# Kernel optimization log

Hardware: AMD Instinct MI355X
Metric: run time of the kernel (lower is better)

The kernel has to match this reference:

```python
import jax, jax.numpy as jnp
import numpy as np

B, N, D, T, L = 16, 64, 4, 40, 10
H, K = 128, 4
E = N * (N - 1)


def setup_inputs() -> dict:
    key = jax.random.key(0)
    ks = jax.random.split(key, 24)
    s = 0.05
    off = np.ones((N, N)) - np.eye(N)
    recv, send = np.where(off)  # rel_rec one-hot of recv, rel_send one-hot of send
    p = {}
    p["data"] = jax.random.normal(ks[0], (B, N, D, T), jnp.float32)
    p["rel_type"] = jax.random.uniform(ks[1], (B, E, K), dtype=jnp.float32)
    p["msg_W1"] = jax.random.normal(ks[2], (K, 2 * H, H), jnp.float32) * s
    p["msg_b1"] = jnp.zeros((K, H), jnp.float32)
    p["msg_W2"] = jax.random.normal(ks[3], (K, H, H), jnp.float32) * s
    p["msg_b2"] = jnp.zeros((K, H), jnp.float32)
    p["Wr_h"] = jax.random.normal(ks[4], (H, H), jnp.float32) * s
    p["Wi_h"] = jax.random.normal(ks[5], (H, H), jnp.float32) * s
    p["Wh_h"] = jax.random.normal(ks[6], (H, H), jnp.float32) * s
    p["Wr_in"] = jax.random.normal(ks[7], (D, H), jnp.float32) * s
    p["br_in"] = jnp.zeros((H,), jnp.float32)
    p["Wi_in"] = jax.random.normal(ks[8], (D, H), jnp.float32) * s
    p["bi_in"] = jnp.zeros((H,), jnp.float32)
    p["Wn_in"] = jax.random.normal(ks[9], (D, H), jnp.float32) * s
    p["bn_in"] = jnp.zeros((H,), jnp.float32)
    p["Wo1"] = jax.random.normal(ks[10], (H, H), jnp.float32) * s
    p["bo1"] = jnp.zeros((H,), jnp.float32)
    p["Wo2"] = jax.random.normal(ks[11], (H, H), jnp.float32) * s
    p["bo2"] = jnp.zeros((H,), jnp.float32)
    p["Wo3"] = jax.random.normal(ks[12], (H, D), jnp.float32) * s
    p["bo3"] = jnp.zeros((D,), jnp.float32)
    p["recv_idx"] = jnp.asarray(recv, jnp.int32)
    p["send_idx"] = jnp.asarray(send, jnp.int32)
    return p


def _forward(data, rel_type, msg_W1, msg_b1, msg_W2, msg_b2, Wr_h, Wi_h, Wh_h,
             Wr_in, br_in, Wi_in, bi_in, Wn_in, bn_in,
             Wo1, bo1, Wo2, bo2, Wo3, bo3, recv_idx, send_idx):
    inputs = jnp.transpose(data, (0, 3, 1, 2))  # [B,T,N,D]
    Bv = inputs.shape[0]

    def single_step(ins, hidden):
        # gather == matmul with one-hot rel_send / rel_rec
        pre_msg = jnp.concatenate([hidden[:, send_idx], hidden[:, recv_idx]], axis=-1)  # [B,E,2H]
        m = jnp.tanh(jnp.einsum('bef,kfh->bkeh', pre_msg, msg_W1) + msg_b1[None, :, None, :])
        m = jnp.tanh(jnp.einsum('bkeh,khg->bkeg', m, msg_W2) + msg_b2[None, :, None, :])
        # sum over edge types weighted by rel_type, normalized by num edge types
        all_msgs = jnp.einsum('bkeh,bek->beh', m, rel_type) / K
        # scatter-add to receivers == rel_rec^T matmul; normalized by n_in_node
        agg = jnp.zeros((Bv, N, H), all_msgs.dtype).at[:, recv_idx].add(all_msgs) / D
        r = jax.nn.sigmoid(ins @ Wr_in + br_in + agg @ Wr_h)
        i = jax.nn.sigmoid(ins @ Wi_in + bi_in + agg @ Wi_h)
        n = jnp.tanh(ins @ Wn_in + bn_in + r * (agg @ Wh_h))
        hidden = (1.0 - i) * n + i * hidden
        y = jax.nn.relu(hidden @ Wo1 + bo1)
        y = jax.nn.relu(y @ Wo2 + bo2)
        pred = ins + y @ Wo3 + bo3
        return pred, hidden

    inputs_pad = jnp.concatenate([inputs, jnp.zeros((Bv, L, N, D), inputs.dtype)], axis=1)
    xs_t = jnp.transpose(inputs_pad, (1, 0, 2, 3))  # [T+L,B,N,D]

    def scan_fn(carry, xs):
        hidden, prev = carry
        step, x_t = xs
        ins = jnp.where(step < T, x_t, prev)  # burn-in then closed-loop
        pred, hidden = single_step(ins, hidden)
        return (hidden, pred), pred

    init = (jnp.zeros((Bv, N, H), jnp.float32), jnp.zeros((Bv, N, D), jnp.float32))
    _, preds = jax.lax.scan(scan_fn, init, (jnp.arange(T + L), xs_t))
    preds = jnp.transpose(preds, (1, 2, 3, 0))  # [B,N,D,T+L]
    return preds[..., -L:]


def reference(data, rel_type, msg_W1, msg_b1, msg_W2, msg_b2, Wr_h, Wi_h, Wh_h,
              Wr_in, br_in, Wi_in, bi_in, Wn_in, bn_in,
              Wo1, bo1, Wo2, bo2, Wo3, bo3, recv_idx, send_idx):
    return _forward(data, rel_type, msg_W1, msg_b1, msg_W2, msg_b2, Wr_h, Wi_h, Wh_h,
                    Wr_in, br_in, Wi_in, bi_in, Wn_in, bn_in,
                    Wo1, bo1, Wo2, bo2, Wo3, bo3, recv_idx, send_idx)
```

## Files before the change

kernel.cpp:

```cpp
#include <hip/hip_runtime.h>
#include <hip/hip_bf16.h>
#include <math.h>

#define Bb 16
#define Nn 64
#define Dd 4
#define Tt 40
#define Ll 10
#define Hh 128
#define Kk 4
#define Ee (Nn*(Nn-1))
#define BNH (Bb*Nn*Hh)
#define SIGMA 2.8853900817779268f

typedef __attribute__((ext_vector_type(8))) short short8;
typedef __attribute__((ext_vector_type(4))) float f32x4;

#define AS1 __attribute__((address_space(1)))
#define AS3 __attribute__((address_space(3)))

__device__ __forceinline__ float tanhE(float y){
    float e = __builtin_amdgcn_exp2f(y);
    float r = __builtin_amdgcn_rcpf(e + 1.0f);
    return fmaf(-2.0f, r, 1.0f);
}
__device__ __forceinline__ float tanh_fast(float x){ return tanhE(SIGMA * x); }
__device__ __forceinline__ float sigmoid_fast(float x){
    return __builtin_amdgcn_rcpf(1.0f + __expf(-x));
}
__device__ __forceinline__ unsigned short f2bf(float x){
    unsigned int u = __float_as_uint(x);
    return (unsigned short)((u + 0x7FFFu + ((u >> 16) & 1u)) >> 16);
}
__device__ __forceinline__ unsigned int pack_bf2(float lo, float hi){
    union { __hip_bfloat162 h; unsigned int u; } cv;
    cv.h = __float22bfloat162_rn(make_float2(lo, hi));
    return cv.u;
}
__device__ __forceinline__ void g2lds16(const void* g, void* l){
    __builtin_amdgcn_global_load_lds((const AS1 unsigned int*)g,
                                     (AS3 unsigned int*)l, 16, 0, 0);
}

__global__ void __launch_bounds__(256) kW2f(const float* __restrict__ W2,
                                            const float* __restrict__ b2,
                                            unsigned short* __restrict__ W2f,
                                            float* __restrict__ b2l){
    if (blockIdx.x == 32){
        int i = threadIdx.x;
        b2l[i]       = SIGMA * b2[i];
        b2l[i + 256] = SIGMA * b2[i + 256];
        return;
    }
    int t    = blockIdx.x * 256 + threadIdx.x;
    int lane = t & 63;
    int nt   = (t >> 6) & 7;
    int kc   = (t >> 9) & 3;
    int k    = (t >> 11) & 3;
    int col  = nt * 16 + (lane & 15);
    int fb   = kc * 32 + (lane >> 4) * 8;
    unsigned int w[4];
#pragma unroll
    for (int p = 0; p < 4; ++p){
        unsigned short lo = f2bf(W2[(k*Hh + fb + 2*p    )*Hh + col]);
        unsigned short hi = f2bf(W2[(k*Hh + fb + 2*p + 1)*Hh + col]);
        w[p] = (unsigned int)lo | ((unsigned int)hi << 16);
    }
    ((uint4*)W2f)[t] = make_uint4(w[0], w[1], w[2], w[3]);
}

__global__ void __launch_bounds__(256) kW1f(const float* __restrict__ W1,
                                            unsigned short* __restrict__ W1f){
    int t    = blockIdx.x * 256 + threadIdx.x;
    int lane = t & 63;
    int nt   = (t >> 6) & 7;
    int kc   = (t >> 9) & 3;
    int s    = t >> 11;
    int col  = nt * 16 + (lane & 15);
    int fb   = kc * 32 + (lane >> 4) * 8;
    unsigned int w[4];
#pragma unroll
    for (int p = 0; p < 4; ++p){
        unsigned short lo = f2bf(W1[(size_t)(s*Hh + fb + 2*p    )*Hh + col]);
        unsigned short hi = f2bf(W1[(size_t)(s*Hh + fb + 2*p + 1)*Hh + col]);
        w[p] = (unsigned int)lo | ((unsigned int)hi << 16);
    }
    ((uint4*)W1f)[t] = make_uint4(w[0], w[1], w[2], w[3]);
}

__global__ void __launch_bounds__(256) kInit(const float* __restrict__ b1,
                                             float* __restrict__ Sf,
                                             float* __restrict__ Rr){
    int i = blockIdx.x*256 + threadIdx.x;
    Sf[i] = 0.0f;
    Rr[i] = SIGMA * b1[((i >> 13) & 3)*Hh + (i & 127)];
}

__global__ void __launch_bounds__(256) kA(const unsigned short* __restrict__ hbf,
                                          const unsigned short* __restrict__ W1f,
                                          const float* __restrict__ b1,
                                          float* __restrict__ Sf,
                                          float* __restrict__ Rr){
    const int blk   = blockIdx.x;
    const int bk    = blk & 63;
    const int b     = bk >> 2;
    const int k     = bk & 3;
    const int inner = blk >> 6;
    const int sr    = inner >> 1;
    const int mh    = inner & 1;
    const int s     = k*2 + sr;
    const int tid  = threadIdx.x;
    const int wave = tid >> 6;
    const int lane = tid & 63;
    const int nt0  = wave * 2;

    const short8* hv = (const short8*)hbf;
    const short8* wv = (const short8*)W1f;

    short8 a[2][4], bf[2][4];
#pragma unroll
    for (int m = 0; m < 2; ++m)
#pragma unroll
        for (int kc = 0; kc < 4; ++kc)
            a[m][kc] = hv[((size_t)((b*4 + mh*2 + m)*4) + kc)*64 + lane];
#pragma unroll
    for (int n = 0; n < 2; ++n)
#pragma unroll
        for (int kc = 0; kc < 4; ++kc)
            bf[n][kc] = wv[((size_t)(s*4 + kc)*8 + nt0 + n)*64 + lane];

    f32x4 acc[2][2];
#pragma unroll
    for (int m = 0; m < 2; ++m){ acc[m][0] = (f32x4)0.0f; acc[m][1] = (f32x4)0.0f; }

#pragma unroll
    for (int kc = 0; kc < 4; ++kc)
#pragma unroll
        for (int m = 0; m < 2; ++m){
            acc[m][0] = __builtin_amdgcn_mfma_f32_16x16x32_bf16(a[m][kc], bf[0][kc], acc[m][0], 0, 0, 0);
            acc[m][1] = __builtin_amdgcn_mfma_f32_16x16x32_bf16(a[m][kc], bf[1][kc], acc[m][1], 0, 0, 0);
        }

    const int col = lane & 15;
    const int r0  = (lane >> 4) << 2;
#pragma unroll
    for (int n = 0; n < 2; ++n){
        const int h  = (nt0 + n)*16 + col;
        const float bv = (sr == 1) ? b1[k*Hh + h] : 0.0f;
#pragma unroll
        for (int m = 0; m < 2; ++m){
            const int Mt = mh*2 + m;
#pragma unroll
            for (int r = 0; r < 4; ++r){
                const int node = Mt*16 + r0 + r;
                const float v = SIGMA*(acc[m][n][r] + bv);
                if (sr == 0)
                    Sf[((size_t)((b*4+k)*16 + (h>>3)))*512 + node*8 + (h&7)] = v;
                else
                    Rr[((size_t)((b*4+k)*64 + node))*128 + h] = v;
            }
        }
    }
}

__global__ void __launch_bounds__(512, 2) kB(const float* __restrict__ Sf,
                                             const float* __restrict__ Rr,
                                             const unsigned short* __restrict__ W2f,
                                             const float* __restrict__ b2l,
                                             const float* __restrict__ rel,
                                             float* __restrict__ aggp){
    __shared__ unsigned short w2s[32*512];
    __shared__ float sfs[8192];
    __shared__ float rrs[8*Hh];
    __shared__ float rel_s[8][64];
    __shared__ float b2s[Hh];

    const int blk  = blockIdx.x;
    const int k    = blk & 3;
    const int no   = (blk >> 2) & 7;
    const int b    = blk >> 5;
    const int tid  = threadIdx.x;
    const int wave = tid >> 6;
    const int lane = tid & 63;

    {
        const uint4* src = (const uint4*)(W2f + (size_t)k*16384);
        uint4* dst = (uint4*)w2s;
#pragma unroll
        for (int i = 0; i < 4; ++i)
            g2lds16(src + tid + i*512, dst + tid + i*512);
    }
    {
        const char* srcB = (const char*)(Sf + (size_t)((b*4 + k)*16)*512);
        char* dstB = (char*)sfs;
#pragma unroll
        for (int i = 0; i < 4; ++i){
            int p = i*8192 + tid*16;
            int g = p ^ (((p >> 11) & 7) << 4);
            g2lds16(srcB + g, dstB + p);
        }
    }
    if (tid < 256){
        const uint4* src = (const uint4*)(Rr + (size_t)((b*4 + k)*64 + no*8)*128);
        g2lds16(src + tid, (uint4*)rrs + tid);
    }
    {
        int g = tid >> 6, s = tid & 63;
        int n = no*8 + g;
        float w = 0.0f;
        if (s != n){
            int e = s - (s > n);
            w = rel[(b*Ee + n*63 + e)*Kk + k];
        }
        rel_s[g][s] = w;
    }
    if (tid < 128) b2s[tid] = b2l[k*Hh + tid];
    __syncthreads();

    const int n     = no*8 + wave;
    const int fo    = lane >> 4;
    const int srow  = lane & 15;
    const char* sfsB = (const char*)sfs;
    const float* rrw = rrs + wave*Hh;
    const short8* w2v = (const short8*)w2s;
    const float* relw = rel_s[wave];

    const int colb  = lane & 15;
    const int rbase = (lane >> 4) << 2;

    float aggacc[8];
#pragma unroll
    for (int nt = 0; nt < 8; ++nt) aggacc[nt] = 0.0f;

#pragma unroll 1
    for (int st = 0; st < 4; ++st){
        short8 a[4];
#pragma unroll
        for (int kc = 0; kc < 4; ++kc){
            const int fg = kc*4 + fo;
            const int A  = fg*2048 + (st*16 + srow)*32;
            const int sw = (fg & 7) << 4;
            float4 s0 = *(const float4*)(sfsB + (A ^ sw));
            float4 s1 = *(const float4*)(sfsB + ((A + 16) ^ sw));
            const float4* rp = (const float4*)(rrw + fg*8);
            float4 r0 = rp[0], r1 = rp[1];
            union { short8 v; unsigned int u[4]; } av;
            av.u[0] = pack_bf2(tanhE(s0.x+r0.x), tanhE(s0.y+r0.y));
            av.u[1] = pack_bf2(tanhE(s0.z+r0.z), tanhE(s0.w+r0.w));
            av.u[2] = pack_bf2(tanhE(s1.x+r1.x), tanhE(s1.y+r1.y));
            av.u[3] = pack_bf2(tanhE(s1.z+r1.z), tanhE(s1.w+r1.w));
            a[kc] = av.v;
        }

        f32x4 acc[8];
#pragma unroll
        for (int nt = 0; nt < 8; ++nt) acc[nt] = (f32x4)0.0f;
#pragma unroll
        for (int kc = 0; kc < 4; ++kc){
#pragma unroll
            for (int nt = 0; nt < 8; ++nt){
                short8 bfr = w2v[(kc*8 + nt)*64 + lane];
                acc[nt] = __builtin_amdgcn_mfma_f32_16x16x32_bf16(a[kc], bfr, acc[nt], 0, 0, 0);
            }
        }

#pragma unroll
        for (int nt = 0; nt < 8; ++nt){
            float bv = b2s[nt*16 + colb];
            float s = 0.0f;
#pragma unroll
            for (int r = 0; r < 4; ++r)
                s = fmaf(relw[st*16 + rbase + r], tanhE(fmaf(SIGMA, acc[nt][r], bv)), s);
            s += __shfl_xor(s, 16);
            s += __shfl_xor(s, 32);
            aggacc[nt] += s;
        }
    }

    if (lane < 16){
#pragma unroll
        for (int nt = 0; nt < 8; ++nt)
            aggp[(size_t)k*BNH + (size_t)(b*64 + n)*Hh + nt*16 + lane] = aggacc[nt];
    }
}

__global__ void __launch_bounds__(128) kC(const float* __restrict__ data,
                                          const float* __restrict__ aggp,
                                          float* __restrict__ hidden,
                                          float* __restrict__ prevpred,
                                          unsigned short* __restrict__ hbf,
                                          const float* __restrict__ Wr_in, const float* __restrict__ br_in,
                                          const float* __restrict__ Wi_in, const float* __restrict__ bi_in,
                                          const float* __restrict__ Wn_in, const float* __restrict__ bn_in,
                                          const float* __restrict__ Wr_h,  const float* __restrict__ Wi_h,
                                          const float* __restrict__ Wh_h,
                                          const float* __restrict__ Wo1,   const float* __restrict__ bo1,
                                          const float* __restrict__ Wo2,   const float* __restrict__ bo2,
                                          const float* __restrict__ Wo3,   const float* __restrict__ bo3,
                                          float* __restrict__ out, int t){
    __shared__ float aggL[4][Hh];
    __shared__ float buf[4][Hh];
    __shared__ float insL[4][Dd];

    const int bn0 = blockIdx.x * 4;
    const int h   = threadIdx.x;

#pragma unroll
    for (int g = 0; g < 4; ++g){
        int bn = bn0 + g;
        aggL[g][h] = (aggp[bn*Hh + h] + aggp[BNH + bn*Hh + h] +
                      aggp[2*BNH + bn*Hh + h] + aggp[3*BNH + bn*Hh + h]) * (1.0f/16.0f);
    }
    if (h < 16){
        int g = h >> 2, d = h & 3;
        int bn = bn0 + g;
        insL[g][d] = (t < Tt) ? data[(bn*Dd + d)*Tt + t] : prevpred[bn*Dd + d];
    }
    __syncthreads();

    float rh[4] = {0,0,0,0}, ih[4] = {0,0,0,0}, hh[4] = {0,0,0,0};
    for (int f = 0; f < Hh; ++f){
        float wr = Wr_h[f*Hh + h], wi = Wi_h[f*Hh + h], wh = Wh_h[f*Hh + h];
#pragma unroll
        for (int g = 0; g < 4; ++g){
            float av = aggL[g][f];
            rh[g] += av*wr; ih[g] += av*wi; hh[g] += av*wh;
        }
    }

    const float wr0 = Wr_in[h],        wr1 = Wr_in[Hh + h],
                wr2 = Wr_in[2*Hh + h], wr3 = Wr_in[3*Hh + h];
    const float wi0 = Wi_in[h],        wi1 = Wi_in[Hh + h],
                wi2 = Wi_in[2*Hh + h], wi3 = Wi_in[3*Hh + h];
    const float wn0 = Wn_in[h],        wn1 = Wn_in[Hh + h],
                wn2 = Wn_in[2*Hh + h], wn3 = Wn_in[3*Hh + h];
    const float brv = br_in[h], biv = bi_in[h], bnv = bn_in[h];

    const int kc  = h >> 5;
    const int lhi = (h >> 3) & 3;
    const int j   = h & 7;

#pragma unroll
    for (int g = 0; g < 4; ++g){
        float i0 = insL[g][0], i1 = insL[g][1], i2 = insL[g][2], i3 = insL[g][3];
        float r  = sigmoid_fast(brv + i0*wr0 + i1*wr1 + i2*wr2 + i3*wr3 + rh[g]);
        float ii = sigmoid_fast(biv + i0*wi0 + i1*wi1 + i2*wi2 + i3*wi3 + ih[g]);
        float nn = tanh_fast   (bnv + i0*wn0 + i1*wn1 + i2*wn2 + i3*wn3 + r*hh[g]);
        float hold = hidden[(bn0+g)*Hh + h];
        float hnew = (1.0f - ii)*nn + ii*hold;
        hidden[(bn0+g)*Hh + h] = hnew;
        buf[g][h] = hnew;
        int bn   = bn0 + g;
        int bb   = bn >> 6, node64 = bn & 63;
        int Mt   = node64 >> 4;
        int lane = (node64 & 15) + lhi*16;
        hbf[((size_t)((bb*4 + Mt)*4 + kc)*64 + lane)*8 + j] = f2bf(hnew);
    }
    __syncthreads();

    float y1[4]; const float b1v = bo1[h];
#pragma unroll
    for (int g = 0; g < 4; ++g) y1[g] = b1v;
    for (int f = 0; f < Hh; ++f){
        float wv = Wo1[f*Hh + h];
#pragma unroll
        for (int g = 0; g < 4; ++g) y1[g] += buf[g][f]*wv;
    }
    __syncthreads();
#pragma unroll
    for (int g = 0; g < 4; ++g) buf[g][h] = fmaxf(y1[g], 0.0f);
    __syncthreads();

    float y2[4]; const float b2v = bo2[h];
#pragma unroll
    for (int g = 0; g < 4; ++g) y2[g] = b2v;
    for (int f = 0; f < Hh; ++f){
        float wv = Wo2[f*Hh + h];
#pragma unroll
        for (int g = 0; g < 4; ++g) y2[g] += buf[g][f]*wv;
    }
    __syncthreads();
#pragma unroll
    for (int g = 0; g < 4; ++g) buf[g][h] = fmaxf(y2[g], 0.0f);
    __syncthreads();

    if (h < 16){
        int g = h >> 2, d = h & 3;
        float pv = bo3[d];
        for (int f = 0; f < Hh; ++f) pv += buf[g][f]*Wo3[f*Dd + d];
        pv += insL[g][d];
        int bn = bn0 + g;
        prevpred[bn*Dd + d] = pv;
        if (t >= Tt) out[(bn*Dd + d)*Ll + (t - Tt)] = pv;
    }
}

extern "C" void kernel_launch(void* const* d_in, const int* in_sizes, int n_in,
                              void* d_out, int out_size, void* d_ws, size_t ws_size,
                              hipStream_t stream){
    const float* data  = (const float*)d_in[0];
    const float* rel   = (const float*)d_in[1];
    const float* W1    = (const float*)d_in[2];
    const float* b1    = (const float*)d_in[3];
    const float* W2    = (const float*)d_in[4];
    const float* b2    = (const float*)d_in[5];
    const float* Wr_h  = (const float*)d_in[6];
    const float* Wi_h  = (const float*)d_in[7];
    const float* Wh_h  = (const float*)d_in[8];
    const float* Wr_in = (const float*)d_in[9];
    const float* br_in = (const float*)d_in[10];
    const float* Wi_in = (const float*)d_in[11];
    const float* bi_in = (const float*)d_in[12];
    const float* Wn_in = (const float*)d_in[13];
    const float* bn_in = (const float*)d_in[14];
    const float* Wo1   = (const float*)d_in[15];
    const float* bo1   = (const float*)d_in[16];
    const float* Wo2   = (const float*)d_in[17];
    const float* bo2   = (const float*)d_in[18];
    const float* Wo3   = (const float*)d_in[19];
    const float* bo3   = (const float*)d_in[20];

    float* out = (float*)d_out;
    float* ws  = (float*)d_ws;

    float* hidden   = ws;
    float* prevpred = hidden + BNH;
    float* Sf       = prevpred + Bb*Nn*Dd;
    float* Rr       = Sf + Bb*Kk*16*Nn*8;
    float* aggp     = Rr + Bb*Kk*Nn*Hh;
    unsigned short* W2f = (unsigned short*)(aggp + 4*BNH);
    float* b2l      = (float*)(W2f + 65536);
    unsigned short* W1f = (unsigned short*)(b2l + 512);
    unsigned short* hbf = W1f + 131072;

    hipMemsetAsync(hidden, 0, (Bb*Nn*Hh + Bb*Nn*Dd)*sizeof(float), stream);
    kW2f<<<33, 256, 0, stream>>>(W2, b2, W2f, b2l);
    kW1f<<<64, 256, 0, stream>>>(W1, W1f);
    kInit<<<2048, 256, 0, stream>>>(b1, Sf, Rr);

    for (int t = 0; t < Tt + Ll; ++t){
        kB<<<512, 512, 0, stream>>>(Sf, Rr, W2f, b2l, rel, aggp);
        kC<<<256, 128, 0, stream>>>(data, aggp, hidden, prevpred, hbf,
                                    Wr_in, br_in, Wi_in, bi_in, Wn_in, bn_in,
                                    Wr_h, Wi_h, Wh_h,
                                    Wo1, bo1, Wo2, bo2, Wo3, bo3, out, t);
        if (t < Tt + Ll - 1)
            kA<<<256, 256, 0, stream>>>(hbf, W1f, b1, Sf, Rr);
    }
}
```

Measured before the change: 2.240 ms.

## Fuse first message-MLP layer into edge kernel and split GRU reductions across threads

Removes the separate kA kernel and the Sf/Rr global buffers. Each kB block now recomputes the sender and receiver projections of the first message layer with MFMA and writes them straight into shared memory, which saves one launch per step and a global round trip. The cost is redundant work: each of the 8 blocks per (b,k) recomputes the full sender projection. kC also doubles its thread count, splitting each 128-wide reduction into two 64-wide halves that are combined through shared memory, at the price of extra barriers.

```diff
diff --git a/kernel.cpp b/kernel.cpp
--- a/kernel.cpp
+++ b/kernel.cpp
@@ -88,84 +88,10 @@
     ((uint4*)W1f)[t] = make_uint4(w[0], w[1], w[2], w[3]);
 }
 
-__global__ void __launch_bounds__(256) kInit(const float* __restrict__ b1,
-                                             float* __restrict__ Sf,
-                                             float* __restrict__ Rr){
-    int i = blockIdx.x*256 + threadIdx.x;
-    Sf[i] = 0.0f;
-    Rr[i] = SIGMA * b1[((i >> 13) & 3)*Hh + (i & 127)];
-}
-
-__global__ void __launch_bounds__(256) kA(const unsigned short* __restrict__ hbf,
-                                          const unsigned short* __restrict__ W1f,
-                                          const float* __restrict__ b1,
-                                          float* __restrict__ Sf,
-                                          float* __restrict__ Rr){
-    const int blk   = blockIdx.x;
-    const int bk    = blk & 63;
-    const int b     = bk >> 2;
-    const int k     = bk & 3;
-    const int inner = blk >> 6;
-    const int sr    = inner >> 1;
-    const int mh    = inner & 1;
-    const int s     = k*2 + sr;
-    const int tid  = threadIdx.x;
-    const int wave = tid >> 6;
-    const int lane = tid & 63;
-    const int nt0  = wave * 2;
-
-    const short8* hv = (const short8*)hbf;
-    const short8* wv = (const short8*)W1f;
-
-    short8 a[2][4], bf[2][4];
-#pragma unroll
-    for (int m = 0; m < 2; ++m)
-#pragma unroll
-        for (int kc = 0; kc < 4; ++kc)
-            a[m][kc] = hv[((size_t)((b*4 + mh*2 + m)*4) + kc)*64 + lane];
-#pragma unroll
-    for (int n = 0; n < 2; ++n)
-#pragma unroll
-        for (int kc = 0; kc < 4; ++kc)
-            bf[n][kc] = wv[((size_t)(s*4 + kc)*8 + nt0 + n)*64 + lane];
-
-    f32x4 acc[2][2];
-#pragma unroll
-    for (int m = 0; m < 2; ++m){ acc[m][0] = (f32x4)0.0f; acc[m][1] = (f32x4)0.0f; }
-
-#pragma unroll
-    for (int kc = 0; kc < 4; ++kc)
-#pragma unroll
-        for (int m = 0; m < 2; ++m){
-            acc[m][0] = __builtin_amdgcn_mfma_f32_16x16x32_bf16(a[m][kc], bf[0][kc], acc[m][0], 0, 0, 0);
-            acc[m][1] = __builtin_amdgcn_mfma_f32_16x16x32_bf16(a[m][kc], bf[1][kc], acc[m][1], 0, 0, 0);
-        }
-
-    const int col = lane & 15;
-    const int r0  = (lane >> 4) << 2;
-#pragma unroll
-    for (int n = 0; n < 2; ++n){
-        const int h  = (nt0 + n)*16 + col;
-        const float bv = (sr == 1) ? b1[k*Hh + h] : 0.0f;
-#pragma unroll
-        for (int m = 0; m < 2; ++m){
-            const int Mt = mh*2 + m;
-#pragma unroll
-            for (int r = 0; r < 4; ++r){
-                const int node = Mt*16 + r0 + r;
-                const float v = SIGMA*(acc[m][n][r] + bv);
-                if (sr == 0)
-                    Sf[((size_t)((b*4+k)*16 + (h>>3)))*512 + node*8 + (h&7)] = v;
-                else
-                    Rr[((size_t)((b*4+k)*64 + node))*128 + h] = v;
-            }
-        }
-    }
-}
-
-__global__ void __launch_bounds__(512, 2) kB(const float* __restrict__ Sf,
-                                             const float* __restrict__ Rr,
+__global__ void __launch_bounds__(512, 2) kB(const unsigned short* __restrict__ hbf,
+                                             const unsigned short* __restrict__ W1f,
                                              const unsigned short* __restrict__ W2f,
+                                             const float* __restrict__ b1,
                                              const float* __restrict__ b2l,
                                              const float* __restrict__ rel,
                                              float* __restrict__ aggp){
@@ -191,20 +117,6 @@
             g2lds16(src + tid + i*512, dst + tid + i*512);
     }
     {
-        const char* srcB = (const char*)(Sf + (size_t)((b*4 + k)*16)*512);
-        char* dstB = (char*)sfs;
-#pragma unroll
-        for (int i = 0; i < 4; ++i){
-            int p = i*8192 + tid*16;
-            int g = p ^ (((p >> 11) & 7) << 4);
-            g2lds16(srcB + g, dstB + p);
-        }
-    }
-    if (tid < 256){
-        const uint4* src = (const uint4*)(Rr + (size_t)((b*4 + k)*64 + no*8)*128);
-        g2lds16(src + tid, (uint4*)rrs + tid);
-    }
-    {
         int g = tid >> 6, s = tid & 63;
         int n = no*8 + g;
         float w = 0.0f;
@@ -215,18 +127,75 @@
         rel_s[g][s] = w;
     }
     if (tid < 128) b2s[tid] = b2l[k*Hh + tid];
-    __syncthreads();
-
-    const int n     = no*8 + wave;
-    const int fo    = lane >> 4;
-    const int srow  = lane & 15;
+
+    const short8* hv = (const short8*)hbf;
+    const short8* wv = (const short8*)W1f;
+    const int colb  = lane & 15;
+    const int rbase = (lane >> 4) << 2;
+
+    {
+        const int mt  = wave >> 1;
+        const int nt0 = (wave & 1) * 4;
+        short8 a[4];
+#pragma unroll
+        for (int kc = 0; kc < 4; ++kc)
+            a[kc] = hv[((size_t)((b*4 + mt)*4) + kc)*64 + lane];
+        f32x4 acc[4];
+#pragma unroll
+        for (int j = 0; j < 4; ++j) acc[j] = (f32x4)0.0f;
+#pragma unroll
+        for (int kc = 0; kc < 4; ++kc){
+#pragma unroll
+            for (int j = 0; j < 4; ++j){
+                short8 bf = wv[((size_t)((2*k)*4 + kc)*8 + nt0 + j)*64 + lane];
+                acc[j] = __builtin_amdgcn_mfma_f32_16x16x32_bf16(a[kc], bf, acc[j], 0, 0, 0);
+            }
+        }
+        char* sfsB = (char*)sfs;
+#pragma unroll
+        for (int j = 0; j < 4; ++j){
+            int h  = (nt0 + j)*16 + colb;
+            int fg = h >> 3, fl = h & 7;
+            int sw = (fg & 7) << 4;
+#pragma unroll
+            for (int r = 0; r < 4; ++r){
+                int node = mt*16 + rbase + r;
+                int A = fg*2048 + node*32 + fl*4;
+                *(float*)(sfsB + (A ^ sw)) = SIGMA * acc[j][r];
+            }
+        }
+    }
+    {
+        const int mtr = no >> 1;
+        short8 a[4];
+#pragma unroll
+        for (int kc = 0; kc < 4; ++kc)
+            a[kc] = hv[((size_t)((b*4 + mtr)*4) + kc)*64 + lane];
+        f32x4 acc = (f32x4)0.0f;
+#pragma unroll
+        for (int kc = 0; kc < 4; ++kc){
+            short8 bf = wv[((size_t)((2*k+1)*4 + kc)*8 + wave)*64 + lane];
+            acc = __builtin_amdgcn_mfma_f32_16x16x32_bf16(a[kc], bf, acc, 0, 0, 0);
+        }
+        const int h   = wave*16 + colb;
+        const float b1v = b1[k*Hh + h];
+        const int lo  = (no & 1) * 8;
+#pragma unroll
+        for (int r = 0; r < 4; ++r){
+            int row = rbase + r;
+            if (row >= lo && row < lo + 8)
+                rrs[(row - lo)*Hh + h] = SIGMA * (acc[r] + b1v);
+        }
+    }
+    __syncthreads();
+
+    const int n    = no*8 + wave;
+    const int fo   = lane >> 4;
+    const int srow = lane & 15;
     const char* sfsB = (const char*)sfs;
     const float* rrw = rrs + wave*Hh;
     const short8* w2v = (const short8*)w2s;
     const float* relw = rel_s[wave];
-
-    const int colb  = lane & 15;
-    const int rbase = (lane >> 4) << 2;
 
     float aggacc[8];
 #pragma unroll
@@ -284,7 +253,7 @@
     }
 }
 
-__global__ void __launch_bounds__(128) kC(const float* __restrict__ data,
+__global__ void __launch_bounds__(256) kC(const float* __restrict__ data,
                                           const float* __restrict__ aggp,
                                           float* __restrict__ hidden,
                                           float* __restrict__ prevpred,
@@ -301,25 +270,29 @@
     __shared__ float aggL[4][Hh];
     __shared__ float buf[4][Hh];
     __shared__ float insL[4][Dd];
+    __shared__ float psh[3][4][Hh];
 
     const int bn0 = blockIdx.x * 4;
-    const int h   = threadIdx.x;
-
-#pragma unroll
-    for (int g = 0; g < 4; ++g){
+    const int tid = threadIdx.x;
+    const int h   = tid & 127;
+    const int fh  = tid >> 7;
+    const int f0  = fh * 64;
+
+    for (int s2 = tid; s2 < 512; s2 += 256){
+        int g = s2 >> 7, hx = s2 & 127;
         int bn = bn0 + g;
-        aggL[g][h] = (aggp[bn*Hh + h] + aggp[BNH + bn*Hh + h] +
-                      aggp[2*BNH + bn*Hh + h] + aggp[3*BNH + bn*Hh + h]) * (1.0f/16.0f);
-    }
-    if (h < 16){
-        int g = h >> 2, d = h & 3;
+        aggL[g][hx] = (aggp[bn*Hh + hx] + aggp[BNH + bn*Hh + hx] +
+                       aggp[2*BNH + bn*Hh + hx] + aggp[3*BNH + bn*Hh + hx]) * (1.0f/16.0f);
+    }
+    if (tid < 16){
+        int g = tid >> 2, d = tid & 3;
         int bn = bn0 + g;
         insL[g][d] = (t < Tt) ? data[(bn*Dd + d)*Tt + t] : prevpred[bn*Dd + d];
     }
     __syncthreads();
 
     float rh[4] = {0,0,0,0}, ih[4] = {0,0,0,0}, hh[4] = {0,0,0,0};
-    for (int f = 0; f < Hh; ++f){
+    for (int f = f0; f < f0 + 64; ++f){
         float wr = Wr_h[f*Hh + h], wi = Wi_h[f*Hh + h], wh = Wh_h[f*Hh + h];
 #pragma unroll
         for (int g = 0; g < 4; ++g){
@@ -327,65 +300,86 @@
             rh[g] += av*wr; ih[g] += av*wi; hh[g] += av*wh;
         }
     }
-
-    const float wr0 = Wr_in[h],        wr1 = Wr_in[Hh + h],
-                wr2 = Wr_in[2*Hh + h], wr3 = Wr_in[3*Hh + h];
-    const float wi0 = Wi_in[h],        wi1 = Wi_in[Hh + h],
-                wi2 = Wi_in[2*Hh + h], wi3 = Wi_in[3*Hh + h];
-    const float wn0 = Wn_in[h],        wn1 = Wn_in[Hh + h],
-                wn2 = Wn_in[2*Hh + h], wn3 = Wn_in[3*Hh + h];
-    const float brv = br_in[h], biv = bi_in[h], bnv = bn_in[h];
-
-    const int kc  = h >> 5;
-    const int lhi = (h >> 3) & 3;
-    const int j   = h & 7;
-
-#pragma unroll
-    for (int g = 0; g < 4; ++g){
-        float i0 = insL[g][0], i1 = insL[g][1], i2 = insL[g][2], i3 = insL[g][3];
-        float r  = sigmoid_fast(brv + i0*wr0 + i1*wr1 + i2*wr2 + i3*wr3 + rh[g]);
-        float ii = sigmoid_fast(biv + i0*wi0 + i1*wi1 + i2*wi2 + i3*wi3 + ih[g]);
-        float nn = tanh_fast   (bnv + i0*wn0 + i1*wn1 + i2*wn2 + i3*wn3 + r*hh[g]);
-        float hold = hidden[(bn0+g)*Hh + h];
-        float hnew = (1.0f - ii)*nn + ii*hold;
-        hidden[(bn0+g)*Hh + h] = hnew;
-        buf[g][h] = hnew;
-        int bn   = bn0 + g;
-        int bb   = bn >> 6, node64 = bn & 63;
-        int Mt   = node64 >> 4;
-        int lane = (node64 & 15) + lhi*16;
-        hbf[((size_t)((bb*4 + Mt)*4 + kc)*64 + lane)*8 + j] = f2bf(hnew);
-    }
-    __syncthreads();
-
-    float y1[4]; const float b1v = bo1[h];
-#pragma unroll
-    for (int g = 0; g < 4; ++g) y1[g] = b1v;
-    for (int f = 0; f < Hh; ++f){
-        float wv = Wo1[f*Hh + h];
-#pragma unroll
-        for (int g = 0; g < 4; ++g) y1[g] += buf[g][f]*wv;
-    }
-    __syncthreads();
-#pragma unroll
-    for (int g = 0; g < 4; ++g) buf[g][h] = fmaxf(y1[g], 0.0f);
-    __syncthreads();
-
-    float y2[4]; const float b2v = bo2[h];
-#pragma unroll
-    for (int g = 0; g < 4; ++g) y2[g] = b2v;
-    for (int f = 0; f < Hh; ++f){
-        float wv = Wo2[f*Hh + h];
-#pragma unroll
-        for (int g = 0; g < 4; ++g) y2[g] += buf[g][f]*wv;
-    }
-    __syncthreads();
-#pragma unroll
-    for (int g = 0; g < 4; ++g) buf[g][h] = fmaxf(y2[g], 0.0f);
-    __syncthreads();
-
-    if (h < 16){
-        int g = h >> 2, d = h & 3;
+    if (fh){
+#pragma unroll
+        for (int g = 0; g < 4; ++g){
+            psh[0][g][h] = rh[g]; psh[1][g][h] = ih[g]; psh[2][g][h] = hh[g];
+        }
+    }
+    __syncthreads();
+
+    if (!fh){
+        const float wr0 = Wr_in[h],        wr1 = Wr_in[Hh + h],
+                    wr2 = Wr_in[2*Hh + h], wr3 = Wr_in[3*Hh + h];
+        const float wi0 = Wi_in[h],        wi1 = Wi_in[Hh + h],
+                    wi2 = Wi_in[2*Hh + h], wi3 = Wi_in[3*Hh + h];
+        const float wn0 = Wn_in[h],        wn1 = Wn_in[Hh + h],
+                    wn2 = Wn_in[2*Hh + h], wn3 = Wn_in[3*Hh + h];
+        const float brv = br_in[h], biv = bi_in[h], bnv = bn_in[h];
+        const int kc  = h >> 5;
+        const int lhi = (h >> 3) & 3;
+        const int j   = h & 7;
+#pragma unroll
+        for (int g = 0; g < 4; ++g){
+            float i0 = insL[g][0], i1 = insL[g][1], i2 = insL[g][2], i3 = insL[g][3];
+            float r  = sigmoid_fast(brv + i0*wr0 + i1*wr1 + i2*wr2 + i3*wr3 + rh[g] + psh[0][g][h]);
+            float ii = sigmoid_fast(biv + i0*wi0 + i1*wi1 + i2*wi2 + i3*wi3 + ih[g] + psh[1][g][h]);
+            float nn = tanh_fast   (bnv + i0*wn0 + i1*wn1 + i2*wn2 + i3*wn3 + r*(hh[g] + psh[2][g][h]));
+            float hold = hidden[(bn0+g)*Hh + h];
+            float hnew = (1.0f - ii)*nn + ii*hold;
+            hidden[(bn0+g)*Hh + h] = hnew;
+            buf[g][h] = hnew;
+            int bn   = bn0 + g;
+            int bb   = bn >> 6, node64 = bn & 63;
+            int Mt   = node64 >> 4;
+            int lane = (node64 & 15) + lhi*16;
+            hbf[((size_t)((bb*4 + Mt)*4 + kc)*64 + lane)*8 + j] = f2bf(hnew);
+        }
+    }
+    __syncthreads();
+
+    {
+        float yp[4] = {0,0,0,0};
+        for (int f = f0; f < f0 + 64; ++f){
+            float wv1 = Wo1[f*Hh + h];
+#pragma unroll
+            for (int g = 0; g < 4; ++g) yp[g] += buf[g][f]*wv1;
+        }
+        if (fh){
+#pragma unroll
+            for (int g = 0; g < 4; ++g) psh[0][g][h] = yp[g];
+        }
+        __syncthreads();
+        if (!fh){
+            float b1v = bo1[h];
+#pragma unroll
+            for (int g = 0; g < 4; ++g) buf[g][h] = fmaxf(b1v + yp[g] + psh[0][g][h], 0.0f);
+        }
+    }
+    __syncthreads();
+
+    {
+        float yp[4] = {0,0,0,0};
+        for (int f = f0; f < f0 + 64; ++f){
+            float wv2 = Wo2[f*Hh + h];
+#pragma unroll
+            for (int g = 0; g < 4; ++g) yp[g] += buf[g][f]*wv2;
+        }
+        if (fh){
+#pragma unroll
+            for (int g = 0; g < 4; ++g) psh[0][g][h] = yp[g];
+        }
+        __syncthreads();
+        if (!fh){
+            float b2v = bo2[h];
+#pragma unroll
+            for (int g = 0; g < 4; ++g) buf[g][h] = fmaxf(b2v + yp[g] + psh[0][g][h], 0.0f);
+        }
+    }
+    __syncthreads();
+
+    if (tid < 16){
+        int g = tid >> 2, d = tid & 3;
         float pv = bo3[d];
         for (int f = 0; f < Hh; ++f) pv += buf[g][f]*Wo3[f*Dd + d];
         pv += insL[g][d];
@@ -425,26 +419,21 @@
 
     float* hidden   = ws;
     float* prevpred = hidden + BNH;
-    float* Sf       = prevpred + Bb*Nn*Dd;
-    float* Rr       = Sf + Bb*Kk*16*Nn*8;
-    float* aggp     = Rr + Bb*Kk*Nn*Hh;
+    unsigned short* hbf = (unsigned short*)(prevpred + Bb*Nn*Dd);
+    float* aggp     = (float*)(hbf + BNH);
     unsigned short* W2f = (unsigned short*)(aggp + 4*BNH);
     float* b2l      = (float*)(W2f + 65536);
     unsigned short* W1f = (unsigned short*)(b2l + 512);
-    unsigned short* hbf = W1f + 131072;
-
-    hipMemsetAsync(hidden, 0, (Bb*Nn*Hh + Bb*Nn*Dd)*sizeof(float), stream);
+
+    hipMemsetAsync(hidden, 0, (size_t)(Bb*Nn*Hh + Bb*Nn*Dd)*4 + (size_t)BNH*2, stream);
     kW2f<<<33, 256, 0, stream>>>(W2, b2, W2f, b2l);
     kW1f<<<64, 256, 0, stream>>>(W1, W1f);
-    kInit<<<2048, 256, 0, stream>>>(b1, Sf, Rr);
 
     for (int t = 0; t < Tt + Ll; ++t){
-        kB<<<512, 512, 0, stream>>>(Sf, Rr, W2f, b2l, rel, aggp);
-        kC<<<256, 128, 0, stream>>>(data, aggp, hidden, prevpred, hbf,
+        kB<<<512, 512, 0, stream>>>(hbf, W1f, W2f, b1, b2l, rel, aggp);
+        kC<<<256, 256, 0, stream>>>(data, aggp, hidden, prevpred, hbf,
                                     Wr_in, br_in, Wi_in, bi_in, Wn_in, bn_in,
                                     Wr_h, Wi_h, Wh_h,
                                     Wo1, bo1, Wo2, bo2, Wo3, bo3, out, t);
-        if (t < Tt + Ll - 1)
-            kA<<<256, 256, 0, stream>>>(hbf, W1f, b1, Sf, Rr);
-    }
-}
+    }
+}
```

Result: faster. 2.174 ms (-2.9%).
